# Optimization experiments

Hardware: AMD Instinct MI355X
Metric: run time of the kernel (lower is better)

## Reference

```python
import jax, jax.numpy as jnp
import numpy as np

S = 14            # grid size, hardcoded via torch.arange(14) in the original
N = S * S         # 196 cells (one box per cell in this implementation)
B = 1024
NUM_CLS = 90
LAMBDA_COORD = 5.0
LAMBDA_NOOBJ = 0.5


def setup_inputs() -> dict:
    key = jax.random.key(0)
    k1, k2, k3 = jax.random.split(key, 3)
    p_yolo = jax.random.uniform(k1, (B, S, S, 5 + NUM_CLS), dtype=jnp.float32)
    g_yolo = jax.random.uniform(k2, (B, S, S, 5 + NUM_CLS), dtype=jnp.float32)
    obj = jax.random.uniform(k3, (B, S, S)) < 0.05
    g_yolo = g_yolo.at[..., 4].set(jnp.where(obj, g_yolo[..., 4], 0.0))
    return {"p_yolo": p_yolo, "g_yolo": g_yolo}


def reference(p_yolo, g_yolo):
    Bc = p_yolo.shape[0]
    dt = p_yolo.dtype
    # which cells contain an object (coo_mask), flattened row-major like torch
    valid = (g_yolo[..., 4] > 0).reshape(Bc, N)          # [B, N] bool
    vf = valid.astype(dt)
    pred = p_yolo[..., :5].reshape(Bc, N, 5)             # [B, N, 5]
    targ = g_yolo[..., :5].reshape(Bc, N, 5)             # [B, N, 5]

    # grid cell coordinates (row-major flatten matches torch boolean-mask order)
    rows = jnp.repeat(jnp.arange(S, dtype=dt), S)        # [N]
    cols = jnp.tile(jnp.arange(S, dtype=dt), S)          # [N]
    # cal_iou converts target xy to global coords IN PLACE before the xy mse
    tx = cols / S + targ[..., 0] / S                     # [B, N]
    ty = rows / S + targ[..., 1] / S
    tw, th = targ[..., 2], targ[..., 3]

    # IoU [B, Npred, Ntarg] -- same math as cal_iou (pred stays in local coords)
    dx = jnp.abs(tx[:, None, :] - pred[:, :, None, 0])
    dy = jnp.abs(ty[:, None, :] - pred[:, :, None, 1])
    sw = (tw[:, None, :] + pred[:, :, None, 2]) * 0.5
    sh = (th[:, None, :] + pred[:, :, None, 3]) * 0.5
    inter = jnp.maximum((sw - dx) * (sh - dy), 0.0)      # clamp after product, as original
    union = (tw * th)[:, None, :] + (pred[..., 2] * pred[..., 3])[:, :, None] - inter
    iou = inter / union

    # per-target best prediction (max over pred dim = dim 0 in original)
    best_iou = iou.max(axis=1)                           # [B, N]
    best_idx = iou.argmax(axis=1)                        # [B, N] int
    bp = jnp.take_along_axis(pred, best_idx[..., None], axis=1)  # [B, N, 5]

    # localization (xy) loss: matched pred xy vs global target xy, sum over valid targets
    xy_loss = jnp.sum(vf * ((bp[..., 0] - tx) ** 2 + (bp[..., 1] - ty) ** 2))

    # confidence loss for matched boxes: (pred_conf * iou - 1)^2
    con_obj_loss = jnp.sum(vf * (bp[..., 4] * best_iou - 1.0) ** 2)

    # no-object confidence loss: preds NOT selected by any valid target,
    # only counted for images that contain at least one object (original skips empty images)
    hit = jnp.zeros((Bc, N), dtype=dt).at[jnp.arange(Bc)[:, None], best_idx].max(vf)
    has_obj = vf.max(axis=1)                             # [B]
    nocon_obj_loss = jnp.sum(has_obj[:, None] * (1.0 - hit) * pred[..., 4] ** 2)

    # class loss over object cells (batched over all images)
    cls_d = (p_yolo[..., 5:] - g_yolo[..., 5:]).reshape(Bc, N, NUM_CLS)
    con_class_loss = jnp.sum(vf[..., None] * cls_d ** 2)

    # NOTE: original total doubles xy_loss and never uses wh_loss -- kept faithful
    total = (LAMBDA_COORD * (xy_loss + xy_loss) + con_obj_loss
             + LAMBDA_NOOBJ * nocon_obj_loss + con_class_loss) / Bc
    return total
```

## Files before the change

### kernel.cpp

```cpp
#include <hip/hip_runtime.h>
#include <math.h>

#define GS 14
#define NCELL 196
#define NCLS 90
#define CH 95

__global__ __launch_bounds__(256) void yolo_loss_fused(
    const float* __restrict__ p, const float* __restrict__ g,
    float* __restrict__ out, float inv_b)
{
    const int b = blockIdx.x;
    const float* pb = p + (size_t)b * NCELL * CH;
    const float* gb = g + (size_t)b * NCELL * CH;

    __shared__ float sp[NCELL][5];
    __shared__ float st[NCELL][5];
    __shared__ int   svalid[NCELL];
    __shared__ unsigned long long smask[4];
    __shared__ int   shit[NCELL];
    __shared__ float sred[4];

    const int tid  = threadIdx.x;
    const int wave = tid >> 6;
    const int lane = tid & 63;

    bool v = false;
    if (tid < NCELL) {
        const float* pr = pb + tid * CH;
        const float* gr = gb + tid * CH;
        float g4 = gr[4];
        #pragma unroll
        for (int j = 0; j < 4; ++j) { sp[tid][j] = pr[j]; st[tid][j] = gr[j]; }
        sp[tid][4] = pr[4];
        st[tid][4] = g4;
        shit[tid] = 0;
        v = g4 > 0.0f;
    }
    const unsigned long long m = __ballot(v);
    if (lane == 0) smask[wave] = m;
    __syncthreads();

    int base = 0;
    #pragma unroll
    for (int w = 0; w < 4; ++w) if (w < wave) base += __popcll(smask[w]);
    const int count = __popcll(smask[0]) + __popcll(smask[1]) +
                      __popcll(smask[2]) + __popcll(smask[3]);
    if (v) {
        const int pos = base + __popcll(m & ((1ull << lane) - 1ull));
        svalid[pos] = tid;
    }
    __syncthreads();

    float xy_acc = 0.0f, con_acc = 0.0f;

    for (int vt = wave; vt < count; vt += 4) {
        const int t = svalid[vt];
        const float tx = __fadd_rn(__fdiv_rn((float)(t % GS), (float)GS),
                                   __fdiv_rn(st[t][0], (float)GS));
        const float ty = __fadd_rn(__fdiv_rn((float)(t / GS), (float)GS),
                                   __fdiv_rn(st[t][1], (float)GS));
        const float tw = st[t][2], th = st[t][3];
        const float twth = __fmul_rn(tw, th);

        float bi = -INFINITY;
        int   bidx = 0x7fffffff;
        for (int pp = lane; pp < NCELL; pp += 64) {
            const float px = sp[pp][0], py = sp[pp][1];
            const float pw = sp[pp][2], ph = sp[pp][3];
            const float dx = fabsf(__fsub_rn(tx, px));
            const float dy = fabsf(__fsub_rn(ty, py));
            const float sw = __fmul_rn(__fadd_rn(tw, pw), 0.5f);
            const float sh = __fmul_rn(__fadd_rn(th, ph), 0.5f);
            const float inter = fmaxf(__fmul_rn(__fsub_rn(sw, dx),
                                                __fsub_rn(sh, dy)), 0.0f);
            const float uni = __fsub_rn(__fadd_rn(twth, __fmul_rn(pw, ph)), inter);
            const float iou = __fdiv_rn(inter, uni);
            if (iou > bi || (iou == bi && pp < bidx)) { bi = iou; bidx = pp; }
        }
        for (int off = 32; off; off >>= 1) {
            const float oi  = __shfl_xor(bi, off);
            const int   oid = __shfl_xor(bidx, off);
            if (oi > bi || (oi == bi && oid < bidx)) { bi = oi; bidx = oid; }
        }
        if (lane == 0) {
            const float d0 = __fsub_rn(sp[bidx][0], tx);
            const float d1 = __fsub_rn(sp[bidx][1], ty);
            xy_acc += __fadd_rn(__fmul_rn(d0, d0), __fmul_rn(d1, d1));
            const float cc = __fsub_rn(__fmul_rn(sp[bidx][4], bi), 1.0f);
            con_acc += __fmul_rn(cc, cc);
            shit[bidx] = 1;
        }
    }
    __syncthreads();

    float nocon_acc = 0.0f;
    if (count > 0 && tid < NCELL) {
        if (!shit[tid]) {
            const float c = sp[tid][4];
            nocon_acc = c * c;
        }
    }

    float cls_acc = 0.0f;
    const int totalc = count * NCLS;
    for (int i = tid; i < totalc; i += 256) {
        const int vt = i / NCLS, j = i - vt * NCLS;
        const int t = svalid[vt];
        const float d = pb[t * CH + 5 + j] - gb[t * CH + 5 + j];
        cls_acc += d * d;
    }

    float tot = 10.0f * xy_acc + con_acc + 0.5f * nocon_acc + cls_acc;
    for (int off = 32; off; off >>= 1) tot += __shfl_xor(tot, off);
    if (lane == 0) sred[wave] = tot;
    __syncthreads();
    if (tid == 0) {
        const float bl = sred[0] + sred[1] + sred[2] + sred[3];
        atomicAdd(out, bl * inv_b);
    }
}

extern "C" void kernel_launch(void* const* d_in, const int* in_sizes, int n_in,
                              void* d_out, int out_size, void* d_ws, size_t ws_size,
                              hipStream_t stream) {
    const float* p = (const float*)d_in[0];
    const float* g = (const float*)d_in[1];
    float* out = (float*)d_out;
    const int B = in_sizes[0] / (NCELL * CH);

    hipMemsetAsync(out, 0, sizeof(float), stream);
    yolo_loss_fused<<<B, 256, 0, stream>>>(p, g, out, 1.0f / (float)B);
}
```

Baseline: 32.44 us.

## Map one image per wavefront with register-resident boxes instead of block-per-image

Each 64-lane wavefront now handles a whole image, with four images per 256-thread block. Box fields sit in registers, the valid-target list comes from ballot masks, and target broadcast uses shuffles, so shared memory and block barriers are gone. Class-score rows are loaded per target inside the same loop. The aim is fewer blocks and less synchronisation and LDS traffic. In exchange, per-target work becomes serial within a wave and more registers are used.

New measurement: 41.45 us. 27.8% more time.

```diff
diff --git a/kernel.cpp b/kernel.cpp
--- a/kernel.cpp
+++ b/kernel.cpp
@@ -6,112 +6,129 @@
 #define NCLS 90
 #define CH 95
 
-__global__ __launch_bounds__(256) void yolo_loss_fused(
+__global__ __launch_bounds__(256) void yolo_loss_wave(
     const float* __restrict__ p, const float* __restrict__ g,
-    float* __restrict__ out, float inv_b)
+    float* __restrict__ out, float inv_b, int B)
 {
-    const int b = blockIdx.x;
-    const float* pb = p + (size_t)b * NCELL * CH;
-    const float* gb = g + (size_t)b * NCELL * CH;
-
-    __shared__ float sp[NCELL][5];
-    __shared__ float st[NCELL][5];
-    __shared__ int   svalid[NCELL];
-    __shared__ unsigned long long smask[4];
-    __shared__ int   shit[NCELL];
-    __shared__ float sred[4];
-
     const int tid  = threadIdx.x;
     const int wave = tid >> 6;
     const int lane = tid & 63;
+    const int b = blockIdx.x * 4 + wave;
 
-    bool v = false;
-    if (tid < NCELL) {
-        const float* pr = pb + tid * CH;
-        const float* gr = gb + tid * CH;
-        float g4 = gr[4];
+    __shared__ float sred[4];
+    float tot = 0.0f;
+
+    if (b < B) {
+        const float* pb = p + (size_t)b * NCELL * CH;
+        const float* gb = g + (size_t)b * NCELL * CH;
+
+        float ppx[4], ppy[4], ppw[4], pph[4], ppc[4];
+        float gtx[4], gty[4], gtw[4], gth[4], gtc[4];
         #pragma unroll
-        for (int j = 0; j < 4; ++j) { sp[tid][j] = pr[j]; st[tid][j] = gr[j]; }
-        sp[tid][4] = pr[4];
-        st[tid][4] = g4;
-        shit[tid] = 0;
-        v = g4 > 0.0f;
-    }
-    const unsigned long long m = __ballot(v);
-    if (lane == 0) smask[wave] = m;
-    __syncthreads();
+        for (int k = 0; k < 4; ++k) {
+            const int c = k * 64 + lane;
+            if (c < NCELL) {
+                const float* pr = pb + c * CH;
+                const float* gr = gb + c * CH;
+                ppx[k] = pr[0]; ppy[k] = pr[1]; ppw[k] = pr[2]; pph[k] = pr[3]; ppc[k] = pr[4];
+                gtx[k] = gr[0]; gty[k] = gr[1]; gtw[k] = gr[2]; gth[k] = gr[3]; gtc[k] = gr[4];
+            } else {
+                ppx[k] = ppy[k] = ppw[k] = pph[k] = ppc[k] = 0.0f;
+                gtx[k] = gty[k] = gtw[k] = gth[k] = gtc[k] = 0.0f;
+            }
+        }
 
-    int base = 0;
-    #pragma unroll
-    for (int w = 0; w < 4; ++w) if (w < wave) base += __popcll(smask[w]);
-    const int count = __popcll(smask[0]) + __popcll(smask[1]) +
-                      __popcll(smask[2]) + __popcll(smask[3]);
-    if (v) {
-        const int pos = base + __popcll(m & ((1ull << lane) - 1ull));
-        svalid[pos] = tid;
-    }
-    __syncthreads();
+        unsigned long long vmask[4];
+        #pragma unroll
+        for (int k = 0; k < 4; ++k) vmask[k] = __ballot(gtc[k] > 0.0f);
+        const int count = __popcll(vmask[0]) + __popcll(vmask[1]) +
+                          __popcll(vmask[2]) + __popcll(vmask[3]);
 
-    float xy_acc = 0.0f, con_acc = 0.0f;
+        float xy_acc = 0.0f, con_acc = 0.0f, cls_acc = 0.0f;
+        int hitmask = 0;
 
-    for (int vt = wave; vt < count; vt += 4) {
-        const int t = svalid[vt];
-        const float tx = __fadd_rn(__fdiv_rn((float)(t % GS), (float)GS),
-                                   __fdiv_rn(st[t][0], (float)GS));
-        const float ty = __fadd_rn(__fdiv_rn((float)(t / GS), (float)GS),
-                                   __fdiv_rn(st[t][1], (float)GS));
-        const float tw = st[t][2], th = st[t][3];
-        const float twth = __fmul_rn(tw, th);
+        #pragma unroll
+        for (int k = 0; k < 4; ++k) {
+            unsigned long long m = vmask[k];
+            while (m) {
+                const int ow0 = (int)__builtin_ctzll(m);
+                m &= m - 1ull;
+                const int t = k * 64 + ow0;
 
-        float bi = -INFINITY;
-        int   bidx = 0x7fffffff;
-        for (int pp = lane; pp < NCELL; pp += 64) {
-            const float px = sp[pp][0], py = sp[pp][1];
-            const float pw = sp[pp][2], ph = sp[pp][3];
-            const float dx = fabsf(__fsub_rn(tx, px));
-            const float dy = fabsf(__fsub_rn(ty, py));
-            const float sw = __fmul_rn(__fadd_rn(tw, pw), 0.5f);
-            const float sh = __fmul_rn(__fadd_rn(th, ph), 0.5f);
-            const float inter = fmaxf(__fmul_rn(__fsub_rn(sw, dx),
-                                                __fsub_rn(sh, dy)), 0.0f);
-            const float uni = __fsub_rn(__fadd_rn(twth, __fmul_rn(pw, ph)), inter);
-            const float iou = __fdiv_rn(inter, uni);
-            if (iou > bi || (iou == bi && pp < bidx)) { bi = iou; bidx = pp; }
+                const float* prow = pb + t * CH + 5;
+                const float* grow = gb + t * CH + 5;
+                const float cp0 = prow[lane];
+                const float cg0 = grow[lane];
+                float cp1 = 0.0f, cg1 = 0.0f;
+                if (lane < NCLS - 64) { cp1 = prow[lane + 64]; cg1 = grow[lane + 64]; }
+
+                const float t0 = __shfl(gtx[k], ow0);
+                const float t1 = __shfl(gty[k], ow0);
+                const float tw = __shfl(gtw[k], ow0);
+                const float th = __shfl(gth[k], ow0);
+                const float tx = __fadd_rn(__fdiv_rn((float)(t % GS), (float)GS),
+                                           __fdiv_rn(t0, (float)GS));
+                const float ty = __fadd_rn(__fdiv_rn((float)(t / GS), (float)GS),
+                                           __fdiv_rn(t1, (float)GS));
+                const float twth = __fmul_rn(tw, th);
+
+                float bi = -INFINITY;
+                int   bidx = 0x7fffffff;
+                #pragma unroll
+                for (int k2 = 0; k2 < 4; ++k2) {
+                    const float pw = ppw[k2], ph = pph[k2];
+                    const float dx = fabsf(__fsub_rn(tx, ppx[k2]));
+                    const float dy = fabsf(__fsub_rn(ty, ppy[k2]));
+                    const float sw = __fmul_rn(__fadd_rn(tw, pw), 0.5f);
+                    const float sh = __fmul_rn(__fadd_rn(th, ph), 0.5f);
+                    const float inter = fmaxf(__fmul_rn(__fsub_rn(sw, dx),
+                                                        __fsub_rn(sh, dy)), 0.0f);
+                    const float uni = __fsub_rn(__fadd_rn(twth, __fmul_rn(pw, ph)), inter);
+                    const float iou = __fdiv_rn(inter, uni);
+                    const bool ok = (k2 < 3) || (lane < NCELL - 192);
+                    const int idx = k2 * 64 + lane;
+                    if (ok && (iou > bi || (iou == bi && idx < bidx))) { bi = iou; bidx = idx; }
+                }
+                #pragma unroll
+                for (int off = 32; off; off >>= 1) {
+                    const float oi  = __shfl_xor(bi, off);
+                    const int   oid = __shfl_xor(bidx, off);
+                    if (oi > bi || (oi == bi && oid < bidx)) { bi = oi; bidx = oid; }
+                }
+                const int ow = bidx & 63, kb = bidx >> 6;
+                if (lane == ow) {
+                    const float bx = kb == 0 ? ppx[0] : kb == 1 ? ppx[1] : kb == 2 ? ppx[2] : ppx[3];
+                    const float by = kb == 0 ? ppy[0] : kb == 1 ? ppy[1] : kb == 2 ? ppy[2] : ppy[3];
+                    const float bc = kb == 0 ? ppc[0] : kb == 1 ? ppc[1] : kb == 2 ? ppc[2] : ppc[3];
+                    const float d0 = __fsub_rn(bx, tx);
+                    const float d1 = __fsub_rn(by, ty);
+                    xy_acc += __fadd_rn(__fmul_rn(d0, d0), __fmul_rn(d1, d1));
+                    const float cc = __fsub_rn(__fmul_rn(bc, bi), 1.0f);
+                    con_acc += __fmul_rn(cc, cc);
+                    hitmask |= 1 << kb;
+                }
+                const float dc0 = cp0 - cg0;
+                const float dc1 = cp1 - cg1;
+                cls_acc += dc0 * dc0 + dc1 * dc1;
+            }
         }
-        for (int off = 32; off; off >>= 1) {
-            const float oi  = __shfl_xor(bi, off);
-            const int   oid = __shfl_xor(bidx, off);
-            if (oi > bi || (oi == bi && oid < bidx)) { bi = oi; bidx = oid; }
+
+        float nocon_acc = 0.0f;
+        if (count > 0) {
+            #pragma unroll
+            for (int k = 0; k < 4; ++k) {
+                const bool cell_ok = (k < 3) || (lane < NCELL - 192);
+                if (cell_ok && !((hitmask >> k) & 1)) {
+                    const float c = ppc[k];
+                    nocon_acc += c * c;
+                }
+            }
         }
-        if (lane == 0) {
-            const float d0 = __fsub_rn(sp[bidx][0], tx);
-            const float d1 = __fsub_rn(sp[bidx][1], ty);
-            xy_acc += __fadd_rn(__fmul_rn(d0, d0), __fmul_rn(d1, d1));
-            const float cc = __fsub_rn(__fmul_rn(sp[bidx][4], bi), 1.0f);
-            con_acc += __fmul_rn(cc, cc);
-            shit[bidx] = 1;
-        }
-    }
-    __syncthreads();
 
-    float nocon_acc = 0.0f;
-    if (count > 0 && tid < NCELL) {
-        if (!shit[tid]) {
-            const float c = sp[tid][4];
-            nocon_acc = c * c;
-        }
+        tot = 10.0f * xy_acc + con_acc + 0.5f * nocon_acc + cls_acc;
     }
 
-    float cls_acc = 0.0f;
-    const int totalc = count * NCLS;
-    for (int i = tid; i < totalc; i += 256) {
-        const int vt = i / NCLS, j = i - vt * NCLS;
-        const int t = svalid[vt];
-        const float d = pb[t * CH + 5 + j] - gb[t * CH + 5 + j];
-        cls_acc += d * d;
-    }
-
-    float tot = 10.0f * xy_acc + con_acc + 0.5f * nocon_acc + cls_acc;
+    #pragma unroll
     for (int off = 32; off; off >>= 1) tot += __shfl_xor(tot, off);
     if (lane == 0) sred[wave] = tot;
     __syncthreads();
@@ -130,5 +147,5 @@
     const int B = in_sizes[0] / (NCELL * CH);
 
     hipMemsetAsync(out, 0, sizeof(float), stream);
-    yolo_loss_fused<<<B, 256, 0, stream>>>(p, g, out, 1.0f / (float)B);
+    yolo_loss_wave<<<(B + 3) / 4, 256, 0, stream>>>(p, g, out, 1.0f / (float)B, B);
 }
```

## Fuse class loss into per-target wave loop with prefetched class rows

Applied to the files above, without the earlier changes.

Box fields are now loaded into shared memory with a flattened cooperative loop across all 256 threads. The svalid compaction is replaced by an iterator over the ballot masks. The class-loss loop is folded into the per-target IoU loop: each wave loads the class rows of its next target while it computes IoU for the current one. This hides class-row load latency behind the IoU work and drops one pass with its integer division. The cost is more register pressure and serialized mask walking in each wave.

New measurement: 35.32 us. 8.9% more time.

```diff
diff --git a/kernel.cpp b/kernel.cpp
--- a/kernel.cpp
+++ b/kernel.cpp
@@ -6,7 +6,7 @@
 #define NCLS 90
 #define CH 95
 
-__global__ __launch_bounds__(256) void yolo_loss_fused(
+__global__ __launch_bounds__(256) void yolo_loss_v8(
     const float* __restrict__ p, const float* __restrict__ g,
     float* __restrict__ out, float inv_b)
 {
@@ -16,7 +16,6 @@
 
     __shared__ float sp[NCELL][5];
     __shared__ float st[NCELL][5];
-    __shared__ int   svalid[NCELL];
     __shared__ unsigned long long smask[4];
     __shared__ int   shit[NCELL];
     __shared__ float sred[4];
@@ -25,37 +24,68 @@
     const int wave = tid >> 6;
     const int lane = tid & 63;
 
-    bool v = false;
-    if (tid < NCELL) {
-        const float* pr = pb + tid * CH;
-        const float* gr = gb + tid * CH;
-        float g4 = gr[4];
-        #pragma unroll
-        for (int j = 0; j < 4; ++j) { sp[tid][j] = pr[j]; st[tid][j] = gr[j]; }
-        sp[tid][4] = pr[4];
-        st[tid][4] = g4;
-        shit[tid] = 0;
-        v = g4 > 0.0f;
+    #pragma unroll
+    for (int it = 0; it < 8; ++it) {
+        const int f = tid + it * 256;
+        if (f < 2 * NCELL * 5) {
+            const int isg = f >= NCELL * 5;
+            const int r   = isg ? f - NCELL * 5 : f;
+            const int c   = r / 5, j = r - c * 5;
+            const float val = (isg ? gb : pb)[c * CH + j];
+            if (isg) st[c][j] = val; else sp[c][j] = val;
+        }
     }
-    const unsigned long long m = __ballot(v);
-    if (lane == 0) smask[wave] = m;
+    if (tid < NCELL) shit[tid] = 0;
     __syncthreads();
 
-    int base = 0;
-    #pragma unroll
-    for (int w = 0; w < 4; ++w) if (w < wave) base += __popcll(smask[w]);
-    const int count = __popcll(smask[0]) + __popcll(smask[1]) +
-                      __popcll(smask[2]) + __popcll(smask[3]);
-    if (v) {
-        const int pos = base + __popcll(m & ((1ull << lane) - 1ull));
-        svalid[pos] = tid;
+    {
+        const int c = wave * 64 + lane;
+        const float cf = (c < NCELL) ? st[c][4] : 0.0f;
+        const unsigned long long m = __ballot(cf > 0.0f);
+        if (lane == 0) smask[wave] = m;
     }
     __syncthreads();
 
-    float xy_acc = 0.0f, con_acc = 0.0f;
+    const unsigned long long m0 = smask[0], m1 = smask[1],
+                             m2 = smask[2], m3 = smask[3];
+    const int count = __popcll(m0) + __popcll(m1) + __popcll(m2) + __popcll(m3);
 
-    for (int vt = wave; vt < count; vt += 4) {
-        const int t = svalid[vt];
+    float xy_acc = 0.0f, con_acc = 0.0f, cls_acc = 0.0f;
+
+    int wk = 0, ord = 0;
+    unsigned long long wm = m0;
+    auto advance = [&]() -> int {
+        for (;;) {
+            while (wm == 0) {
+                if (++wk > 3) return -1;
+                wm = wk == 1 ? m1 : wk == 2 ? m2 : m3;
+            }
+            const int bit = (int)__builtin_ctzll(wm);
+            wm &= wm - 1ull;
+            if (((ord++) & 3) == wave) return wk * 64 + bit;
+        }
+    };
+
+    int t_cur = advance();
+    float cp0 = 0.0f, cg0 = 0.0f, cp1 = 0.0f, cg1 = 0.0f;
+    if (t_cur >= 0) {
+        const float* prow = pb + t_cur * CH + 5;
+        const float* grow = gb + t_cur * CH + 5;
+        cp0 = prow[lane]; cg0 = grow[lane];
+        if (lane < NCLS - 64) { cp1 = prow[lane + 64]; cg1 = grow[lane + 64]; }
+    }
+
+    while (t_cur >= 0) {
+        const int t_nxt = advance();
+        float np0 = 0.0f, ng0 = 0.0f, np1 = 0.0f, ng1 = 0.0f;
+        if (t_nxt >= 0) {
+            const float* prow = pb + t_nxt * CH + 5;
+            const float* grow = gb + t_nxt * CH + 5;
+            np0 = prow[lane]; ng0 = grow[lane];
+            if (lane < NCLS - 64) { np1 = prow[lane + 64]; ng1 = grow[lane + 64]; }
+        }
+
+        const int t = t_cur;
         const float tx = __fadd_rn(__fdiv_rn((float)(t % GS), (float)GS),
                                    __fdiv_rn(st[t][0], (float)GS));
         const float ty = __fadd_rn(__fdiv_rn((float)(t / GS), (float)GS),
@@ -78,6 +108,7 @@
             const float iou = __fdiv_rn(inter, uni);
             if (iou > bi || (iou == bi && pp < bidx)) { bi = iou; bidx = pp; }
         }
+        #pragma unroll
         for (int off = 32; off; off >>= 1) {
             const float oi  = __shfl_xor(bi, off);
             const int   oid = __shfl_xor(bidx, off);
@@ -91,6 +122,13 @@
             con_acc += __fmul_rn(cc, cc);
             shit[bidx] = 1;
         }
+
+        const float dc0 = cp0 - cg0;
+        const float dc1 = cp1 - cg1;
+        cls_acc += dc0 * dc0 + dc1 * dc1;
+
+        cp0 = np0; cg0 = ng0; cp1 = np1; cg1 = ng1;
+        t_cur = t_nxt;
     }
     __syncthreads();
 
@@ -102,16 +140,8 @@
         }
     }
 
-    float cls_acc = 0.0f;
-    const int totalc = count * NCLS;
-    for (int i = tid; i < totalc; i += 256) {
-        const int vt = i / NCLS, j = i - vt * NCLS;
-        const int t = svalid[vt];
-        const float d = pb[t * CH + 5 + j] - gb[t * CH + 5 + j];
-        cls_acc += d * d;
-    }
-
     float tot = 10.0f * xy_acc + con_acc + 0.5f * nocon_acc + cls_acc;
+    #pragma unroll
     for (int off = 32; off; off >>= 1) tot += __shfl_xor(tot, off);
     if (lane == 0) sred[wave] = tot;
     __syncthreads();
@@ -130,5 +160,5 @@
     const int B = in_sizes[0] / (NCELL * CH);
 
     hipMemsetAsync(out, 0, sizeof(float), stream);
-    yolo_loss_fused<<<B, 256, 0, stream>>>(p, g, out, 1.0f / (float)B);
+    yolo_loss_v8<<<B, 256, 0, stream>>>(p, g, out, 1.0f / (float)B);
 }
```
